# Optimization experiments

Measured on AMD Instinct MI355X. Metric: run time of the kernel, lower is better.

The kernel has to match this reference:

```python
import jax, jax.numpy as jnp
import numpy as np
import math

FEAT_DIM, M, K = 512, 64, 256
D = FEAT_DIM // M  # 8
ALPHA = 1.0
B = 16384


def setup_inputs() -> dict:
    key = jax.random.key(0)
    kx, kc = jax.random.split(key)
    x = jax.random.normal(kx, (B, FEAT_DIM), dtype=jnp.float32)
    # Codebook: unit-norm codewords scaled by 1/sqrt(M), mimicking the
    # normalized-hypersphere init (orthogonal rotation / permutation do not
    # change the math, only the values).
    c = jax.random.normal(kc, (M, K, D), dtype=jnp.float32)
    c = c / jnp.linalg.norm(c, axis=-1, keepdims=True) / math.sqrt(M)
    return {"x": x, "C": c}


def reference(x, C):
    # x: (B, feat_dim) -> (B, M, D)
    x_ = x.reshape(x.shape[0], M, D)
    # per-subspace inner products with codewords: (B, M, K)
    ips = jnp.einsum('bmd,mkd->bmk', x_, C)
    # training-mode straight-through assignment
    soft = jax.nn.softmax(ips * (M / ALPHA), axis=-1)
    hard = jax.nn.one_hot(jnp.argmax(ips, axis=-1), K, dtype=ips.dtype)
    codes = jax.lax.stop_gradient(hard - soft) + soft
    # reconstruction: (B, M, D) -> (B, feat_dim)
    x_hat = jnp.einsum('mkd,bmk->bmd', C, codes).reshape(x.shape[0], -1)
    return x_hat, codes
```

## Files before the change

### kernel.cpp

```cpp
#include <hip/hip_runtime.h>
#include <math.h>


#define B_SZ   16384
#define FEAT   512
#define M_SZ   64
#define K_SZ   256
#define D_SZ   8

typedef float v4f __attribute__((ext_vector_type(4)));

__global__ __launch_bounds__(256) void pq_fused(
    const float* __restrict__ x,
    const float* __restrict__ C,
    float* __restrict__ xhat,
    float* __restrict__ codes)
{
#pragma clang fp contract(off)

    const int t     = threadIdx.x;
    const int m     = blockIdx.x & (M_SZ - 1);
    const int chunk = blockIdx.x >> 6;
    const int b     = (chunk << 8) | t;

    __shared__ v4f Cs[K_SZ * 2];
    __shared__ unsigned char lbk[256];

    {
        const v4f* src = (const v4f*)(C + (size_t)m * (K_SZ * D_SZ)) + (t << 1);
        Cs[(t << 1) | 0] = src[0];
        Cs[(t << 1) | 1] = src[1];
    }

    const float* xp = x + (size_t)b * FEAT + m * D_SZ;
    const v4f xa = ((const v4f*)xp)[0];
    const v4f xb = ((const v4f*)xp)[1];

    __syncthreads();

    float best  = -INFINITY;
    int   bestk = 0;

#pragma unroll 4
    for (int k = 0; k < K_SZ; ++k) {
        const v4f ca = Cs[(k << 1) | 0];
        const v4f cb = Cs[(k << 1) | 1];
        v4f P = xa * ca;
        v4f Q = xb * cb;
        v4f T = P + Q;
        float dot = (T.x + T.y) + (T.z + T.w);
        if (dot > best) { best = dot; bestk = k; }
    }

    {
        const v4f h0 = Cs[(bestk << 1) | 0];
        const v4f h1 = Cs[(bestk << 1) | 1];
        float* xh = xhat + (size_t)b * FEAT + m * D_SZ;
        ((v4f*)xh)[0] = h0;
        ((v4f*)xh)[1] = h1;
    }

    lbk[t] = (unsigned char)bestk;
    __syncthreads();

    const int w     = t >> 6;
    const int lane  = t & 63;
    const int lane4 = lane << 2;

#pragma unroll 4
    for (int j = 0; j < 64; ++j) {
        const int i  = (j << 2) | w;
        const int kk = (int)lbk[i];
        float4 v;
        v.x = (kk == lane4 + 0) ? 1.0f : 0.0f;
        v.y = (kk == lane4 + 1) ? 1.0f : 0.0f;
        v.z = (kk == lane4 + 2) ? 1.0f : 0.0f;
        v.w = (kk == lane4 + 3) ? 1.0f : 0.0f;
        const size_t f4 = ((size_t)((chunk << 8) | i) << 12) + (m << 6) + lane;
        ((float4*)codes)[f4] = v;
    }
}

extern "C" void kernel_launch(void* const* d_in, const int* in_sizes, int n_in,
                              void* d_out, int out_size, void* d_ws, size_t ws_size,
                              hipStream_t stream)
{
    const float* x = (const float*)d_in[0];
    const float* C = (const float*)d_in[1];
    float* xhat  = (float*)d_out;
    float* codes = (float*)d_out + (size_t)B_SZ * FEAT;

    hipLaunchKernelGGL(pq_fused, dim3(4096), dim3(256), 0, stream,
                       x, C, xhat, codes);
}
```

Before: 1.149 ms.

## Process four batch rows per thread to reuse codebook LDS reads

Each thread now computes argmax over the codebook for four batch rows instead of one. Each pair of codeword vectors read from shared memory is reused for four dot products, and the grid shrinks by four. The aim is to cut LDS traffic and per-block setup such as the codebook load and barriers per row. The cost is higher register pressure and fewer blocks (four per CU), which may reduce latency hiding in the large one-hot codes write phase.

```diff
diff --git a/kernel.cpp b/kernel.cpp
--- a/kernel.cpp
+++ b/kernel.cpp
@@ -21,10 +21,10 @@
     const int t     = threadIdx.x;
     const int m     = blockIdx.x & (M_SZ - 1);
     const int chunk = blockIdx.x >> 6;
-    const int b     = (chunk << 8) | t;
+    const int base  = (chunk << 10) | t;
 
     __shared__ v4f Cs[K_SZ * 2];
-    __shared__ unsigned char lbk[256];
+    __shared__ unsigned char lbk[1024];
 
     {
         const v4f* src = (const v4f*)(C + (size_t)m * (K_SZ * D_SZ)) + (t << 1);
@@ -32,35 +32,60 @@
         Cs[(t << 1) | 1] = src[1];
     }
 
-    const float* xp = x + (size_t)b * FEAT + m * D_SZ;
-    const v4f xa = ((const v4f*)xp)[0];
-    const v4f xb = ((const v4f*)xp)[1];
+    const float* xp0 = x + (size_t)base * FEAT + m * D_SZ;
+    const float* xp1 = xp0 + (size_t)256 * FEAT;
+    const float* xp2 = xp1 + (size_t)256 * FEAT;
+    const float* xp3 = xp2 + (size_t)256 * FEAT;
+    const v4f xa0 = ((const v4f*)xp0)[0], xb0 = ((const v4f*)xp0)[1];
+    const v4f xa1 = ((const v4f*)xp1)[0], xb1 = ((const v4f*)xp1)[1];
+    const v4f xa2 = ((const v4f*)xp2)[0], xb2 = ((const v4f*)xp2)[1];
+    const v4f xa3 = ((const v4f*)xp3)[0], xb3 = ((const v4f*)xp3)[1];
 
     __syncthreads();
 
-    float best  = -INFINITY;
-    int   bestk = 0;
+    float best0 = -INFINITY, best1 = -INFINITY;
+    float best2 = -INFINITY, best3 = -INFINITY;
+    int   bk0 = 0, bk1 = 0, bk2 = 0, bk3 = 0;
 
-#pragma unroll 4
+#pragma unroll 2
     for (int k = 0; k < K_SZ; ++k) {
         const v4f ca = Cs[(k << 1) | 0];
         const v4f cb = Cs[(k << 1) | 1];
-        v4f P = xa * ca;
-        v4f Q = xb * cb;
-        v4f T = P + Q;
-        float dot = (T.x + T.y) + (T.z + T.w);
-        if (dot > best) { best = dot; bestk = k; }
+
+        v4f P0 = xa0 * ca, Q0 = xb0 * cb, T0 = P0 + Q0;
+        float d0 = (T0.x + T0.y) + (T0.z + T0.w);
+        v4f P1 = xa1 * ca, Q1 = xb1 * cb, T1 = P1 + Q1;
+        float d1 = (T1.x + T1.y) + (T1.z + T1.w);
+        v4f P2 = xa2 * ca, Q2 = xb2 * cb, T2 = P2 + Q2;
+        float d2 = (T2.x + T2.y) + (T2.z + T2.w);
+        v4f P3 = xa3 * ca, Q3 = xb3 * cb, T3 = P3 + Q3;
+        float d3 = (T3.x + T3.y) + (T3.z + T3.w);
+
+        if (d0 > best0) { best0 = d0; bk0 = k; }
+        if (d1 > best1) { best1 = d1; bk1 = k; }
+        if (d2 > best2) { best2 = d2; bk2 = k; }
+        if (d3 > best3) { best3 = d3; bk3 = k; }
     }
 
     {
-        const v4f h0 = Cs[(bestk << 1) | 0];
-        const v4f h1 = Cs[(bestk << 1) | 1];
-        float* xh = xhat + (size_t)b * FEAT + m * D_SZ;
-        ((v4f*)xh)[0] = h0;
-        ((v4f*)xh)[1] = h1;
+        float* xh0 = xhat + (size_t)base * FEAT + m * D_SZ;
+        ((v4f*)xh0)[0] = Cs[(bk0 << 1) | 0];
+        ((v4f*)xh0)[1] = Cs[(bk0 << 1) | 1];
+        float* xh1 = xh0 + (size_t)256 * FEAT;
+        ((v4f*)xh1)[0] = Cs[(bk1 << 1) | 0];
+        ((v4f*)xh1)[1] = Cs[(bk1 << 1) | 1];
+        float* xh2 = xh1 + (size_t)256 * FEAT;
+        ((v4f*)xh2)[0] = Cs[(bk2 << 1) | 0];
+        ((v4f*)xh2)[1] = Cs[(bk2 << 1) | 1];
+        float* xh3 = xh2 + (size_t)256 * FEAT;
+        ((v4f*)xh3)[0] = Cs[(bk3 << 1) | 0];
+        ((v4f*)xh3)[1] = Cs[(bk3 << 1) | 1];
     }
 
-    lbk[t] = (unsigned char)bestk;
+    lbk[t]       = (unsigned char)bk0;
+    lbk[t + 256] = (unsigned char)bk1;
+    lbk[t + 512] = (unsigned char)bk2;
+    lbk[t + 768] = (unsigned char)bk3;
     __syncthreads();
 
     const int w     = t >> 6;
@@ -68,7 +93,7 @@
     const int lane4 = lane << 2;
 
 #pragma unroll 4
-    for (int j = 0; j < 64; ++j) {
+    for (int j = 0; j < 256; ++j) {
         const int i  = (j << 2) | w;
         const int kk = (int)lbk[i];
         float4 v;
@@ -76,7 +101,7 @@
         v.y = (kk == lane4 + 1) ? 1.0f : 0.0f;
         v.z = (kk == lane4 + 2) ? 1.0f : 0.0f;
         v.w = (kk == lane4 + 3) ? 1.0f : 0.0f;
-        const size_t f4 = ((size_t)((chunk << 8) | i) << 12) + (m << 6) + lane;
+        const size_t f4 = ((size_t)((chunk << 10) | i) << 12) + (m << 6) + lane;
         ((float4*)codes)[f4] = v;
     }
 }
@@ -90,6 +115,6 @@
     float* xhat  = (float*)d_out;
     float* codes = (float*)d_out + (size_t)B_SZ * FEAT;
 
-    hipLaunchKernelGGL(pq_fused, dim3(4096), dim3(256), 0, stream,
+    hipLaunchKernelGGL(pq_fused, dim3(1024), dim3(256), 0, stream,
                        x, C, xhat, codes);
 }
```

Result: no change. 1.152 ms (+0.2%).

## Process four row chunks per block and interleave argmax with code stores

Applied to the files above, without the earlier changes.

Each block now handles 1024 rows in four passes instead of 256. The codebook is loaded into LDS once per block rather than once per 256 rows, and the grid shrinks fourfold. The one-hot code stores for pass p are issued before the argmax of pass p+1, so the store traffic can overlap with compute. In exchange the kernel holds more x registers, uses a larger lbk buffer and has fewer blocks to spread across the GPU. The one-hot output writes (16384x64x256 floats) likely dominate, which limits how much this can help.

```diff
diff --git a/kernel.cpp b/kernel.cpp
--- a/kernel.cpp
+++ b/kernel.cpp
@@ -21,10 +21,12 @@
     const int t     = threadIdx.x;
     const int m     = blockIdx.x & (M_SZ - 1);
     const int chunk = blockIdx.x >> 6;
-    const int b     = (chunk << 8) | t;
+    const int w     = t >> 6;
+    const int lane  = t & 63;
+    const int lane4 = lane << 2;
 
-    __shared__ v4f Cs[K_SZ * 2];
-    __shared__ unsigned char lbk[256];
+    __shared__ v4f           Cs[K_SZ * 2];
+    __shared__ unsigned char lbk[4 * 256];
 
     {
         const v4f* src = (const v4f*)(C + (size_t)m * (K_SZ * D_SZ)) + (t << 1);
@@ -32,53 +34,88 @@
         Cs[(t << 1) | 1] = src[1];
     }
 
-    const float* xp = x + (size_t)b * FEAT + m * D_SZ;
-    const v4f xa = ((const v4f*)xp)[0];
-    const v4f xb = ((const v4f*)xp)[1];
+#define XLOAD(p, XA, XB)                                                        \
+    const float* xp##p = x + ((size_t)((chunk << 10) | (p << 8) | t)) * FEAT    \
+                           + m * D_SZ;                                          \
+    const v4f XA = ((const v4f*)xp##p)[0];                                      \
+    const v4f XB = ((const v4f*)xp##p)[1];
+    XLOAD(0, xa0, xb0)
+    XLOAD(1, xa1, xb1)
+    XLOAD(2, xa2, xb2)
+    XLOAD(3, xa3, xb3)
+#undef XLOAD
 
     __syncthreads();
 
-    float best  = -INFINITY;
-    int   bestk = 0;
-
-#pragma unroll 4
-    for (int k = 0; k < K_SZ; ++k) {
-        const v4f ca = Cs[(k << 1) | 0];
-        const v4f cb = Cs[(k << 1) | 1];
-        v4f P = xa * ca;
-        v4f Q = xb * cb;
-        v4f T = P + Q;
-        float dot = (T.x + T.y) + (T.z + T.w);
-        if (dot > best) { best = dot; bestk = k; }
+#define ARGMAX(XA, XB, BK)                                                      \
+    int BK;                                                                     \
+    {                                                                           \
+        float best = -INFINITY; int bk_ = 0;                                    \
+        _Pragma("unroll 4")                                                     \
+        for (int k = 0; k < K_SZ; ++k) {                                        \
+            const v4f ca = Cs[(k << 1) | 0];          \
+            const v4f cb = Cs[(k << 1) | 1];                                    \
+            v4f P = (XA) * ca;                             \
+            v4f Q = (XB) * cb;                                                  \
+            v4f T = P + Q;                                 \
+            float dot = (T.x + T.y) + (T.z + T.w);                 \
+            if (dot > best) { best = dot; bk_ = k; }   \
+        }                                                                       \
+        BK = bk_;                                                               \
     }
 
-    {
-        const v4f h0 = Cs[(bestk << 1) | 0];
-        const v4f h1 = Cs[(bestk << 1) | 1];
-        float* xh = xhat + (size_t)b * FEAT + m * D_SZ;
-        ((v4f*)xh)[0] = h0;
-        ((v4f*)xh)[1] = h1;
+#define XHAT(p, BK)                                                             \
+    {                                                                           \
+        float* xh = xhat + ((size_t)((chunk << 10) | (p << 8) | t)) * FEAT      \
+                         + m * D_SZ;                                            \
+        ((v4f*)xh)[0] = Cs[(BK << 1) | 0];                                      \
+        ((v4f*)xh)[1] = Cs[(BK << 1) | 1];                                      \
     }
 
-    lbk[t] = (unsigned char)bestk;
+#define STORES(p)                                                               \
+    {                                                                           \
+        const size_t rowbase = (size_t)((chunk << 10) | (p << 8));              \
+        _Pragma("unroll 4")                                                     \
+        for (int j = 0; j < 64; ++j) {                                          \
+            const int i  = (j << 2) | w;                                        \
+            const int kk = (int)lbk[(p << 8) | i];           \
+            float4 v;                                                           \
+            v.x = (kk == lane4 + 0) ? 1.0f : 0.0f;                              \
+            v.y = (kk == lane4 + 1) ? 1.0f : 0.0f;                              \
+            v.z = (kk == lane4 + 2) ? 1.0f : 0.0f;                              \
+            v.w = (kk == lane4 + 3) ? 1.0f : 0.0f;                              \
+            ((float4*)codes)[((rowbase + i) << 12) + (m << 6) + lane] = v;      \
+        }                                                                       \
+    }
+
+    ARGMAX(xa0, xb0, bk0)
+    XHAT(0, bk0)
+    lbk[(0 << 8) | t] = (unsigned char)bk0;
     __syncthreads();
 
-    const int w     = t >> 6;
-    const int lane  = t & 63;
-    const int lane4 = lane << 2;
+    STORES(0)
+    ARGMAX(xa1, xb1, bk1)
+    XHAT(1, bk1)
+    lbk[(1 << 8) | t] = (unsigned char)bk1;
+    __syncthreads();
 
-#pragma unroll 4
-    for (int j = 0; j < 64; ++j) {
-        const int i  = (j << 2) | w;
-        const int kk = (int)lbk[i];
-        float4 v;
-        v.x = (kk == lane4 + 0) ? 1.0f : 0.0f;
-        v.y = (kk == lane4 + 1) ? 1.0f : 0.0f;
-        v.z = (kk == lane4 + 2) ? 1.0f : 0.0f;
-        v.w = (kk == lane4 + 3) ? 1.0f : 0.0f;
-        const size_t f4 = ((size_t)((chunk << 8) | i) << 12) + (m << 6) + lane;
-        ((float4*)codes)[f4] = v;
-    }
+    STORES(1)
+    ARGMAX(xa2, xb2, bk2)
+    XHAT(2, bk2)
+    lbk[(2 << 8) | t] = (unsigned char)bk2;
+    __syncthreads();
+
+    STORES(2)
+    ARGMAX(xa3, xb3, bk3)
+    XHAT(3, bk3)
+    lbk[(3 << 8) | t] = (unsigned char)bk3;
+    __syncthreads();
+
+    STORES(3)
+
+#undef ARGMAX
+#undef XHAT
+#undef STORES
 }
 
 extern "C" void kernel_launch(void* const* d_in, const int* in_sizes, int n_in,
@@ -90,6 +127,6 @@
     float* xhat  = (float*)d_out;
     float* codes = (float*)d_out + (size_t)B_SZ * FEAT;
 
-    hipLaunchKernelGGL(pq_fused, dim3(4096), dim3(256), 0, stream,
+    hipLaunchKernelGGL(pq_fused, dim3(1024), dim3(256), 0, stream,
                        x, C, xhat, codes);
 }
```

Result: no change. 1.154 ms (+0.4%).
